# Optimization experiments

Measured on AMD Instinct MI355X. Metric: run time of the kernel, lower is better.

## Reference

```python
import jax, jax.numpy as jnp
import numpy as np

T, B, I, H, O, L = 256, 128, 128, 512, 1, 5


def setup_inputs() -> dict:
    key = jax.random.key(0)
    ks = jax.random.split(key, 12)
    k = 1.0 / np.sqrt(H)
    u = lambda kk, shape: jax.random.uniform(kk, shape, jnp.float32, -k, k)
    inp = {
        "input_seq": jax.random.normal(ks[0], (T, B, I), jnp.float32),
        # layer 0: input size I, 2 directions
        "W_ih0": u(ks[1], (2, 3 * H, I)),
        "W_hh0": u(ks[2], (2, 3 * H, H)),
        "b_ih0": u(ks[3], (2, 3 * H)),
        "b_hh0": u(ks[4], (2, 3 * H)),
        # layers 1..4: input size 2H, 2 directions
        "W_ih": u(ks[5], (L - 1, 2, 3 * H, 2 * H)),
        "W_hh": u(ks[6], (L - 1, 2, 3 * H, H)),
        "b_ih": u(ks[7], (L - 1, 2, 3 * H)),
        "b_hh": u(ks[8], (L - 1, 2, 3 * H)),
        "fc_w": u(ks[9], (O, 2 * H)),
        "fc_b": u(ks[10], (O,)),
    }
    return inp


def _gru_dir(x, Wih, Whh, bih, bhh):
    # x: [T, B, in]; precompute input-side gates for all timesteps
    gx = jnp.einsum('tbi,gi->tbg', x, Wih) + bih  # [T, B, 3H]

    def step(h, g):
        gh = h @ Whh.T + bhh  # [B, 3H]
        xr, xz, xn = jnp.split(g, 3, axis=-1)
        hr, hz, hn = jnp.split(gh, 3, axis=-1)
        r = jax.nn.sigmoid(xr + hr)
        z = jax.nn.sigmoid(xz + hz)
        n = jnp.tanh(xn + r * hn)
        h_new = (1.0 - z) * n + z * h
        return h_new, h_new

    h0 = jnp.zeros((x.shape[1], Whh.shape[1]), x.dtype)
    _, hs = jax.lax.scan(step, h0, gx)
    return hs  # [T, B, H]


def _bigru_layer(x, Wih, Whh, bih, bhh):
    # Wih: [2, 3H, in]; direction 0 = forward, 1 = backward (PyTorch convention)
    fwd = _gru_dir(x, Wih[0], Whh[0], bih[0], bhh[0])
    bwd = _gru_dir(x[::-1], Wih[1], Whh[1], bih[1], bhh[1])[::-1]
    return jnp.concatenate([fwd, bwd], axis=-1)  # [T, B, 2H]


def reference(input_seq, W_ih0, W_hh0, b_ih0, b_hh0, W_ih, W_hh, b_ih, b_hh, fc_w, fc_b):
    # 5-layer bidirectional GRU (eval mode: inter-layer dropout inactive)
    h = _bigru_layer(input_seq, W_ih0, W_hh0, b_ih0, b_hh0)
    for l in range(L - 1):
        h = _bigru_layer(h, W_ih[l], W_hh[l], b_ih[l], b_hh[l])
    out = jnp.einsum('tbh,oh->tbo', h, fc_w) + fc_b
    return jax.nn.sigmoid(out)
```

## Files before the change

### kernel.cpp

```cpp
#include <hip/hip_runtime.h>
#include <hip/hip_bf16.h>

#define T_ 256
#define B_ 128
#define H_ 512
#define G3 1536
#define SCH 32
#define NCH 8
#define RWG 32
#define BGRP 8

typedef __attribute__((ext_vector_type(8))) short short8;
typedef __attribute__((ext_vector_type(4))) short short4v;
typedef __attribute__((ext_vector_type(4))) float f32x4;
typedef __attribute__((ext_vector_type(4))) unsigned int uint4v;

static __device__ __forceinline__ float b2f(short s){
    unsigned u = ((unsigned)(unsigned short)s) << 16;
    return __builtin_bit_cast(float, u);
}
static __device__ __forceinline__ short f2b(float f){
    __hip_bfloat16 h = __float2bfloat16(f);
    return __builtin_bit_cast(short, h);
}
static __device__ __forceinline__ void gload16(const void* g, void* l){
    __builtin_amdgcn_global_load_lds(
        (__attribute__((address_space(1))) void*)(void*)g,
        (__attribute__((address_space(3))) void*)l, 16, 0, 0);
}
static __device__ __forceinline__ void wait_vm0(){
    asm volatile("s_waitcnt vmcnt(0)" ::: "memory");
}
static __device__ __forceinline__ short8 gload_sc(const short* p){
    short8 v;
    asm volatile("global_load_dwordx4 %0, %1, off sc0 sc1"
                 : "=v"(v) : "v"(p) : "memory");
    return v;
}
static __device__ __forceinline__ void gstore16_sc(short* p, short8 v){
    asm volatile("global_store_dwordx4 %0, %1, off sc0 sc1"
                 :: "v"(p), "v"(v) : "memory");
}
static __device__ __forceinline__ void store_flag(unsigned int* p, unsigned int v){
    asm volatile("global_store_dword %0, %1, off sc0 sc1"
                 :: "v"(p), "v"(v) : "memory");
}
static __device__ __forceinline__ void load_flags8(const unsigned int* p, unsigned int* f){
    uint4v a, b;
    asm volatile("global_load_dwordx4 %0, %2, off sc0 sc1\n\t"
                 "global_load_dwordx4 %1, %3, off sc0 sc1\n\t"
                 "s_waitcnt vmcnt(0)"
                 : "=v"(a), "=v"(b) : "v"(p), "v"(p + 4) : "memory");
    f[0]=a.x; f[1]=a.y; f[2]=a.z; f[3]=a.w;
    f[4]=b.x; f[5]=b.y; f[6]=b.z; f[7]=b.w;
}

__global__ void cvt_f32_to_bf16(const float* __restrict__ src, short* __restrict__ dst, int n){
    int i = (blockIdx.x * blockDim.x + threadIdx.x) * 4;
    int stride = gridDim.x * blockDim.x * 4;
    for (; i + 3 < n; i += stride){
        float4 v = *(const float4*)(src + i);
        short4v o;
        o[0] = f2b(v.x); o[1] = f2b(v.y); o[2] = f2b(v.z); o[3] = f2b(v.w);
        *(short4v*)(dst + i) = o;
    }
}

__global__ __launch_bounds__(256) void gx_gemm(
    const short* __restrict__ A,
    const short* __restrict__ W,
    const float* __restrict__ bias,
    short* __restrict__ gxc,
    int K, int t0f, int t0b_lo)
{
    __shared__ __align__(16) short sA[4096];
    __shared__ __align__(16) short sB[4096];
    const int dir = blockIdx.z;
    const int t0 = dir ? t0b_lo : t0f;
    const int m0 = blockIdx.x * 128;
    const int n0 = blockIdx.y * 128;
    const short* Ae = A + (size_t)(t0 * B_) * K;
    const short* We = W + (size_t)dir * G3 * K;
    short* out = gxc + (size_t)dir * ((size_t)SCH * B_ * G3);

    const int tid = threadIdx.x, wv = tid >> 6, lane = tid & 63;
    const int moff = (wv & 1) * 64, noff = (wv >> 1) * 64;
    const int e0 = wv * 1024 + lane * 8, e1 = e0 + 512;
    const short* a0 = Ae + (size_t)(m0 + (e0 >> 5)) * K + (e0 & 31);
    const short* a1 = Ae + (size_t)(m0 + (e1 >> 5)) * K + (e1 & 31);
    const short* b0 = We + (size_t)(n0 + (e0 >> 5)) * K + (e0 & 31);
    const short* b1 = We + (size_t)(n0 + (e1 >> 5)) * K + (e1 & 31);
    short* sa0 = &sA[wv * 1024];  short* sa1 = &sA[wv * 1024 + 512];
    short* sb0 = &sB[wv * 1024];  short* sb1 = &sB[wv * 1024 + 512];

    f32x4 acc[4][4] = {};
    const int lr = lane & 15, lk = (lane >> 4) * 8;

    for (int kk = 0; kk < K; kk += 32){
        gload16(a0 + kk, sa0); gload16(a1 + kk, sa1);
        gload16(b0 + kk, sb0); gload16(b1 + kk, sb1);
        __syncthreads();
        short8 ar[4], br[4];
        #pragma unroll
        for (int i = 0; i < 4; ++i) ar[i] = *(const short8*)&sA[(moff + i*16 + lr) * 32 + lk];
        #pragma unroll
        for (int i = 0; i < 4; ++i) br[i] = *(const short8*)&sB[(noff + i*16 + lr) * 32 + lk];
        #pragma unroll
        for (int ai = 0; ai < 4; ++ai)
            #pragma unroll
            for (int bi = 0; bi < 4; ++bi)
                acc[ai][bi] = __builtin_amdgcn_mfma_f32_16x16x32_bf16(ar[ai], br[bi], acc[ai][bi], 0, 0, 0);
        __syncthreads();
    }

    #pragma unroll
    for (int ai = 0; ai < 4; ++ai){
        #pragma unroll
        for (int bi = 0; bi < 4; ++bi){
            int col = n0 + noff + bi*16 + lr;
            float bv = bias[dir * G3 + col];
            #pragma unroll
            for (int r = 0; r < 4; ++r){
                int row = m0 + moff + ai*16 + ((lane >> 4) << 2) + r;
                out[(size_t)row * G3 + col] = f2b(acc[ai][bi][r] + bv);
            }
        }
    }
}

__global__ __launch_bounds__(256, 1) void rec_kernel(
    const short* __restrict__ gxc,
    const short* __restrict__ Whh,
    const float* __restrict__ bhh,
    short* __restrict__ xout,
    float* __restrict__ hfm,
    short* __restrict__ hbb,
    unsigned int* __restrict__ flags,
    int t0f, int t0b_hi, int first, int base)
{
    __shared__ __align__(16) short lds_h[32 * 520];
    __shared__ __align__(16) short lds_out[32 * 72];
    const int tid = threadIdx.x, wv = tid >> 6, lane = tid & 63;
    const int ug = blockIdx.x >> 2, bg = blockIdx.x & 3, dir = blockIdx.y;
    const int u0w = ug * 64;
    const int u0 = u0w + wv * 16;
    const int m0 = bg * 32;
    const int lr = lane & 15, lk = (lane >> 4) * 8;
    const int crow = (lane >> 4) * 4;
    const int srow = tid >> 3, scol0 = (tid & 7) * 8;

    const short* Wd = Whh + (size_t)dir * G3 * H_;
    short8 wreg[3][16];
    #pragma unroll
    for (int g = 0; g < 3; ++g)
        #pragma unroll
        for (int kk = 0; kk < 16; ++kk)
            wreg[g][kk] = *(const short8*)&Wd[(size_t)(g*H_ + u0 + lr) * H_ + kk*32 + lk];

    float bh[3];
    #pragma unroll
    for (int g = 0; g < 3; ++g) bh[g] = bhh[dir*G3 + g*H_ + u0 + lr];

    float hreg[2][4];
    #pragma unroll
    for (int mt = 0; mt < 2; ++mt)
        #pragma unroll
        for (int r = 0; r < 4; ++r)
            hreg[mt][r] = first ? 0.f
                : hfm[((size_t)dir*B_ + m0 + mt*16 + crow + r)*H_ + u0 + lr];

    unsigned int* flg = flags + (dir*4 + bg) * 32;
    const short* gxd = gxc + (size_t)dir * ((size_t)SCH * B_ * G3);

    float gv[3][2][4];
    {
        const int tl0 = dir ? (SCH - 1) : 0;
        const short* gb = gxd + ((size_t)(tl0 * B_) + m0 + crow) * G3 + u0 + lr;
        #pragma unroll
        for (int g = 0; g < 3; ++g)
            #pragma unroll
            for (int mt = 0; mt < 2; ++mt)
                #pragma unroll
                for (int r = 0; r < 4; ++r)
                    gv[g][mt][r] = b2f(gb[(size_t)(mt*16 + r) * G3 + g * H_]);
    }

    for (int sl = 0; sl < SCH; ++sl){
        const int sg = base + sl;
        const int t  = dir ? (t0b_hi - sl) : (t0f + sl);
        const int rp = sg & 1;

        if (tid == 0){
            unsigned int f[8];
            for (;;){
                load_flags8(flg, f);
                bool ok = true;
                #pragma unroll
                for (int j = 0; j < 8; ++j) ok &= (f[j] >= (unsigned int)sg);
                if (ok) break;
                __builtin_amdgcn_s_sleep(1);
            }
        }
        __syncthreads();

        {
            const short* hsrc = hbb + ((size_t)(rp*2 + dir) * B_ + m0) * H_;
            short8 hv[8];
            #pragma unroll
            for (int c = 0; c < 8; ++c)
                hv[c] = gload_sc(hsrc + (size_t)srow * H_ + scol0 + c*64);
            wait_vm0();
            #pragma unroll
            for (int c = 0; c < 8; ++c)
                *(short8*)&lds_h[srow * 520 + scol0 + c*64] = hv[c];
        }
        __syncthreads();

        f32x4 acc[3][2] = {};
        #pragma unroll
        for (int kk = 0; kk < 16; ++kk){
            short8 a0 = *(const short8*)&lds_h[(lr)      * 520 + kk*32 + lk];
            short8 a1 = *(const short8*)&lds_h[(16 + lr) * 520 + kk*32 + lk];
            #pragma unroll
            for (int g = 0; g < 3; ++g){
                acc[g][0] = __builtin_amdgcn_mfma_f32_16x16x32_bf16(a0, wreg[g][kk], acc[g][0], 0, 0, 0);
                acc[g][1] = __builtin_amdgcn_mfma_f32_16x16x32_bf16(a1, wreg[g][kk], acc[g][1], 0, 0, 0);
            }
        }

        #pragma unroll
        for (int mt = 0; mt < 2; ++mt){
            #pragma unroll
            for (int r = 0; r < 4; ++r){
                float gr = acc[0][mt][r] + bh[0] + gv[0][mt][r];
                float gz = acc[1][mt][r] + bh[1] + gv[1][mt][r];
                float gn = acc[2][mt][r] + bh[2];
                float xn = gv[2][mt][r];
                float rg = 1.f / (1.f + __expf(-gr));
                float zg = 1.f / (1.f + __expf(-gz));
                float e2 = __expf(2.f * (xn + rg * gn));
                float ng = 1.f - 2.f / (e2 + 1.f);
                float hn = (1.f - zg) * ng + zg * hreg[mt][r];
                hreg[mt][r] = hn;
                lds_out[(mt*16 + crow + r) * 72 + wv*16 + lr] = f2b(hn);
            }
        }
        __syncthreads();

        {
            short8 ov = *(const short8*)&lds_out[srow * 72 + scol0];
            short* hwr = hbb + ((size_t)((rp^1)*2 + dir) * B_ + m0 + srow) * H_ + u0w + scol0;
            gstore16_sc(hwr, ov);
            *(short8*)&xout[((size_t)t * B_ + m0 + srow) * 1024 + dir*H_ + u0w + scol0] = ov;
        }

        wait_vm0();
        __syncthreads();
        if (tid == 0) store_flag(&flg[ug], (unsigned int)(sg + 1));

        if (sl + 1 < SCH){
            const int tln = dir ? (SCH - 2 - sl) : (sl + 1);
            const short* gb = gxd + ((size_t)(tln * B_) + m0 + crow) * G3 + u0 + lr;
            #pragma unroll
            for (int g = 0; g < 3; ++g)
                #pragma unroll
                for (int mt = 0; mt < 2; ++mt)
                    #pragma unroll
                    for (int r = 0; r < 4; ++r)
                        gv[g][mt][r] = b2f(gb[(size_t)(mt*16 + r) * G3 + g * H_]);
        }
    }

    #pragma unroll
    for (int mt = 0; mt < 2; ++mt)
        #pragma unroll
        for (int r = 0; r < 4; ++r)
            hfm[((size_t)dir*B_ + m0 + mt*16 + crow + r)*H_ + u0 + lr] = hreg[mt][r];
}

__global__ void fc_kernel(const short* __restrict__ h, const float* __restrict__ w,
                          const float* __restrict__ b, float* __restrict__ out){
    int wid = threadIdx.x >> 6, lane = threadIdx.x & 63;
    int tb = blockIdx.x * 4 + wid;
    const short* hp = h + (size_t)tb * 1024 + lane * 16;
    float s = 0.f;
    #pragma unroll
    for (int c = 0; c < 2; ++c){
        short8 v = *(const short8*)(hp + c * 8);
        #pragma unroll
        for (int e = 0; e < 8; ++e) s += b2f(v[e]) * w[lane * 16 + c * 8 + e];
    }
    #pragma unroll
    for (int o = 32; o; o >>= 1) s += __shfl_down(s, o);
    if (lane == 0) out[tb] = 1.f / (1.f + __expf(-(s + b[0])));
}

extern "C" void kernel_launch(void* const* d_in, const int* in_sizes, int n_in,
                              void* d_out, int out_size, void* d_ws, size_t ws_size,
                              hipStream_t stream){
    const float* input_seq = (const float*)d_in[0];
    const float* W_ih0 = (const float*)d_in[1];
    const float* W_hh0 = (const float*)d_in[2];
    const float* b_ih0 = (const float*)d_in[3];
    const float* b_hh0 = (const float*)d_in[4];
    const float* W_ih  = (const float*)d_in[5];
    const float* W_hh  = (const float*)d_in[6];
    const float* b_ih  = (const float*)d_in[7];
    const float* b_hh  = (const float*)d_in[8];
    const float* fc_w  = (const float*)d_in[9];
    const float* fc_b  = (const float*)d_in[10];
    (void)in_sizes; (void)n_in; (void)out_size; (void)ws_size;

    char* ws = (char*)d_ws;
    size_t off = 0;
    auto alloc = [&](size_t bytes) -> char* {
        char* p = ws + off; off += (bytes + 255) & ~(size_t)255; return p;
    };
    short* actA = (short*)alloc((size_t)T_*B_*1024 * 2);
    short* actB = (short*)alloc((size_t)T_*B_*1024 * 2);
    short* gxc  = (short*)alloc((size_t)2*SCH*B_*G3 * 2);
    short* wihl = (short*)alloc((size_t)2*G3*1024 * 2);
    short* whhl = (short*)alloc((size_t)2*G3*H_ * 2);
    float* hfm  = (float*)alloc((size_t)2*B_*H_ * 4);
    short* hbb  = (short*)alloc((size_t)2*2*B_*H_ * 2);
    unsigned int* bar = (unsigned int*)alloc(4096);

    auto cvt = [&](const float* s, short* d, size_t n){
        int blocks = (int)((n/4 + 255) / 256); if (blocks > 4096) blocks = 4096;
        hipLaunchKernelGGL(cvt_f32_to_bf16, dim3(blocks), dim3(256), 0, stream, s, d, (int)n);
    };

    cvt(input_seq, actB, (size_t)T_*B_*128);

    for (int l = 0; l < 5; ++l){
        const int K = l ? 1024 : 128;
        cvt(l ? W_ih + (size_t)(l-1)*2*G3*1024 : W_ih0, wihl, (size_t)2*G3*K);
        cvt(l ? W_hh + (size_t)(l-1)*2*G3*H_   : W_hh0, whhl, (size_t)2*G3*H_);
        const short* IN  = (l & 1) ? actA : actB;
        short*       OUT = (l & 1) ? actB : actA;
        const float* bi = l ? b_ih + (size_t)(l-1)*2*G3 : b_ih0;
        const float* bh = l ? b_hh + (size_t)(l-1)*2*G3 : b_hh0;

        hipMemsetAsync(hbb, 0, (size_t)2*2*B_*H_*2, stream);
        hipMemsetAsync(bar, 0, 4096, stream);

        for (int q = 0; q < NCH; ++q){
            const int t0f    = SCH * q;
            const int t0b_hi = T_ - 1 - SCH * q;
            const int t0b_lo = t0b_hi - SCH + 1;
            hipLaunchKernelGGL(gx_gemm, dim3(SCH*B_/128, G3/128, 2), dim3(256), 0, stream,
                               IN, wihl, bi, gxc, K, t0f, t0b_lo);
            hipLaunchKernelGGL(rec_kernel, dim3(RWG, 2), dim3(256), 0, stream,
                               gxc, whhl, bh, OUT, hfm, hbb, bar, t0f, t0b_hi, q == 0, q*SCH);
        }
    }
    hipLaunchKernelGGL(fc_kernel, dim3((T_*B_)/4), dim3(256), 0, stream,
                       actA, fc_w, fc_b, (float*)d_out);
}
```

Measured before the change: 6.539 ms.

## Poll per-producer flags in every thread and defer xout store past flag release

Replaces the single-thread spin on all eight producer flags plus a block barrier with per-thread polling: each thread waits only on the flag of the producer workgroup whose h slice it loads, and the load layout is remapped so each thread reads a contiguous 64-column chunk owned by one producer. The layer-output store to xout is moved after the flag release, so the flag no longer waits on that write. The intent is to shorten the critical path of the recurrent cross-workgroup handoff. In exchange, every thread now issues polling loads, which adds memory traffic, and the sleep between polls is gone.

```diff
diff --git a/kernel.cpp b/kernel.cpp
--- a/kernel.cpp
+++ b/kernel.cpp
@@ -45,14 +45,11 @@
     asm volatile("global_store_dword %0, %1, off sc0 sc1"
                  :: "v"(p), "v"(v) : "memory");
 }
-static __device__ __forceinline__ void load_flags8(const unsigned int* p, unsigned int* f){
-    uint4v a, b;
-    asm volatile("global_load_dwordx4 %0, %2, off sc0 sc1\n\t"
-                 "global_load_dwordx4 %1, %3, off sc0 sc1\n\t"
-                 "s_waitcnt vmcnt(0)"
-                 : "=v"(a), "=v"(b) : "v"(p), "v"(p + 4) : "memory");
-    f[0]=a.x; f[1]=a.y; f[2]=a.z; f[3]=a.w;
-    f[4]=b.x; f[5]=b.y; f[6]=b.z; f[7]=b.w;
+static __device__ __forceinline__ unsigned int poll_dw(const unsigned int* p){
+    unsigned int v;
+    asm volatile("global_load_dword %0, %1, off sc0 sc1\n\ts_waitcnt vmcnt(0)"
+                 : "=v"(v) : "v"(p) : "memory");
+    return v;
 }
 
 __global__ void cvt_f32_to_bf16(const float* __restrict__ src, short* __restrict__ dst, int n){
@@ -147,7 +144,9 @@
     const int m0 = bg * 32;
     const int lr = lane & 15, lk = (lane >> 4) * 8;
     const int crow = (lane >> 4) * 4;
-    const int srow = tid >> 3, scol0 = (tid & 7) * 8;
+    const int srow = tid >> 3;
+    const int pj   = tid & 7;
+    const int scol0 = pj * 8;
 
     const short* Wd = Whh + (size_t)dir * G3 * H_;
     short8 wreg[3][16];
@@ -190,29 +189,17 @@
         const int t  = dir ? (t0b_hi - sl) : (t0f + sl);
         const int rp = sg & 1;
 
-        if (tid == 0){
-            unsigned int f[8];
-            for (;;){
-                load_flags8(flg, f);
-                bool ok = true;
-                #pragma unroll
-                for (int j = 0; j < 8; ++j) ok &= (f[j] >= (unsigned int)sg);
-                if (ok) break;
-                __builtin_amdgcn_s_sleep(1);
-            }
-        }
-        __syncthreads();
-
         {
-            const short* hsrc = hbb + ((size_t)(rp*2 + dir) * B_ + m0) * H_;
+            while (poll_dw(flg + pj) < (unsigned int)sg) { }
+            const short* hsrc = hbb + ((size_t)(rp*2 + dir) * B_ + m0 + srow) * H_ + pj*64;
             short8 hv[8];
             #pragma unroll
             for (int c = 0; c < 8; ++c)
-                hv[c] = gload_sc(hsrc + (size_t)srow * H_ + scol0 + c*64);
+                hv[c] = gload_sc(hsrc + c*8);
             wait_vm0();
             #pragma unroll
             for (int c = 0; c < 8; ++c)
-                *(short8*)&lds_h[srow * 520 + scol0 + c*64] = hv[c];
+                *(short8*)&lds_h[srow * 520 + pj*64 + c*8] = hv[c];
         }
         __syncthreads();
 
@@ -247,16 +234,17 @@
         }
         __syncthreads();
 
+        short8 ov = *(const short8*)&lds_out[srow * 72 + scol0];
         {
-            short8 ov = *(const short8*)&lds_out[srow * 72 + scol0];
             short* hwr = hbb + ((size_t)((rp^1)*2 + dir) * B_ + m0 + srow) * H_ + u0w + scol0;
             gstore16_sc(hwr, ov);
-            *(short8*)&xout[((size_t)t * B_ + m0 + srow) * 1024 + dir*H_ + u0w + scol0] = ov;
         }
 
         wait_vm0();
         __syncthreads();
         if (tid == 0) store_flag(&flg[ug], (unsigned int)(sg + 1));
+
+        *(short8*)&xout[((size_t)t * B_ + m0 + srow) * 1024 + dir*H_ + u0w + scol0] = ov;
 
         if (sl + 1 < SCH){
             const int tln = dir ? (SCH - 2 - sl) : (sl + 1);
```

Measured after the change: 7.718 ms. +18.0%, slower.
